# Kernel optimization log

Hardware: AMD Instinct MI355X
Metric: run time of the kernel (lower is better)

The kernel has to match this reference:

```python
import jax, jax.numpy as jnp
import numpy as np

N, D = 8192, 128

def setup_inputs() -> dict:
    key = jax.random.key(0)
    kq, kk, kv = jax.random.split(key, 3)
    query = jax.random.normal(kq, (N, D), dtype=jnp.float32)
    key_t = jax.random.normal(kk, (N, D), dtype=jnp.float32)
    value = jax.random.normal(kv, (N, D), dtype=jnp.float32)
    return {"query": query, "key": key_t, "value": value}

def reference(query, key, value):
    # FlashAttention-2 online softmax over blocks is mathematically exact
    # softmax attention: out = softmax(Q K^T / sqrt(d)) V, no mask.
    d = query.shape[-1]
    scale = 1.0 / jnp.sqrt(jnp.asarray(d, dtype=query.dtype))
    scores = jnp.einsum('qd,kd->qk', query, key) * scale  # [n, n]
    probs = jax.nn.softmax(scores, axis=-1)
    return jnp.einsum('qk,kd->qd', probs, value)  # [n, d]
```

## Files before the change

### kernel.cpp

```cpp
#include <hip/hip_runtime.h>
#include <hip/hip_bf16.h>

#define ATTN_N 8192
#define ATTN_D 128
#define TKEYS 128
#define NTILES (ATTN_N / TKEYS)
#define TILE_ELEMS (TKEYS * ATTN_D)
#define QROWS 64
#define KTPB 32

typedef __bf16 bf16_t;
typedef bf16_t bf16x2 __attribute__((ext_vector_type(2)));
typedef bf16_t bf16x8 __attribute__((ext_vector_type(8)));
typedef float f32x4 __attribute__((ext_vector_type(4)));

#if __has_builtin(__builtin_amdgcn_exp2f)
#define EXP2(x) __builtin_amdgcn_exp2f(x)
#else
#define EXP2(x) __expf((x) * 0.6931471805599453f)
#endif

__device__ __forceinline__ void dma16(const bf16_t* g, bf16_t* l) {
  __builtin_amdgcn_global_load_lds(
      (const __attribute__((address_space(1))) void*)g,
      (__attribute__((address_space(3))) void*)l, 16, 0, 0);
}

__global__ void prep_kernel(const float* __restrict__ q,
                            const float* __restrict__ k,
                            const float* __restrict__ v,
                            bf16_t* __restrict__ qb,
                            bf16_t* __restrict__ kswz,
                            bf16_t* __restrict__ vtswz) {
  __shared__ bf16_t tile[64][72];
  const int bk = blockIdx.x;
  const int bd = blockIdx.y;
  const int t = threadIdx.x;
  const float sc = 0.12751744f;

  const int row_l = t >> 2;
  const int key = bk * 64 + row_l;
  const int kt = key >> 7;
  const int r = key & 127;

#pragma unroll
  for (int u = 0; u < 2; ++u) {
    const int j = bd * 8 + (t & 3) * 2 + u;
    const float4* qs = (const float4*)(q + (size_t)key * ATTN_D + j * 8);
    const float4* ks = (const float4*)(k + (size_t)key * ATTN_D + j * 8);
    float4 a0 = qs[0], a1 = qs[1];
    float4 b0 = ks[0], b1 = ks[1];
    bf16x8 qo, ko;
    qo[0] = (bf16_t)(a0.x * sc); qo[1] = (bf16_t)(a0.y * sc);
    qo[2] = (bf16_t)(a0.z * sc); qo[3] = (bf16_t)(a0.w * sc);
    qo[4] = (bf16_t)(a1.x * sc); qo[5] = (bf16_t)(a1.y * sc);
    qo[6] = (bf16_t)(a1.z * sc); qo[7] = (bf16_t)(a1.w * sc);
    ko[0] = (bf16_t)b0.x; ko[1] = (bf16_t)b0.y;
    ko[2] = (bf16_t)b0.z; ko[3] = (bf16_t)b0.w;
    ko[4] = (bf16_t)b1.x; ko[5] = (bf16_t)b1.y;
    ko[6] = (bf16_t)b1.z; ko[7] = (bf16_t)b1.w;
    *(bf16x8*)(qb + (size_t)key * ATTN_D + j * 8) = qo;
    *(bf16x8*)(kswz + (size_t)kt * TILE_ELEMS + r * ATTN_D + (j ^ (r & 15)) * 8) = ko;
  }

  {
    const float* src = v + (size_t)key * ATTN_D + bd * 64 + (t & 3) * 16;
#pragma unroll
    for (int u = 0; u < 4; ++u) {
      float4 a = ((const float4*)src)[u];
      tile[row_l][(t & 3) * 16 + u * 4 + 0] = (bf16_t)a.x;
      tile[row_l][(t & 3) * 16 + u * 4 + 1] = (bf16_t)a.y;
      tile[row_l][(t & 3) * 16 + u * 4 + 2] = (bf16_t)a.z;
      tile[row_l][(t & 3) * 16 + u * 4 + 3] = (bf16_t)a.w;
    }
  }
  __syncthreads();
  {
    const int d_l = t >> 2;
    const int d = bd * 64 + d_l;
    const int h = bk & 1;
    const int ktv = bk >> 1;
#pragma unroll
    for (int u = 0; u < 2; ++u) {
      const int j = 8 * h + (t & 3) * 2 + u;
      bf16x8 o;
#pragma unroll
      for (int i = 0; i < 8; ++i) {
        const int key_tile = (j >> 2) * 32 + 4 * (j & 3) + (i >> 1) + 16 * (i & 1);
        o[i] = tile[key_tile - h * 64][d_l];
      }
      *(bf16x8*)(vtswz + (size_t)ktv * TILE_ELEMS + d * TKEYS + (j ^ (d & 15)) * 8) = o;
    }
  }
}

__global__ __launch_bounds__(512) void flash_attn_kernel(
    const bf16_t* __restrict__ qb, const bf16_t* __restrict__ kswz,
    const bf16_t* __restrict__ vtswz, float* __restrict__ partO,
    float* __restrict__ partL) {
  __shared__ __align__(16) bf16_t KV[2][2][TILE_ELEMS];
  __shared__ __align__(16) bf16_t Ps[8][32][40];
  __shared__ float cmb[8][32];
  float* Ob = (float*)&KV[0][0][0];

  const int t = threadIdx.x;
  const int w = t >> 6;
  const int lane = t & 63;
  const int quad = lane >> 4;
  const int col = lane & 15;
  const int rowHalf = w & 1;
  const int keyQ = w >> 1;
  const int blk = blockIdx.x;
  const int qg = blk >> 1;
  const int kh = blk & 1;
  const int q0 = qg * QROWS;
  const int ktbase = kh * KTPB;
  const int stg = ((blk >> 3) & 3) * 8;

  int offK[4][2], offV[8];
#pragma unroll
  for (int c = 0; c < 4; ++c)
#pragma unroll
    for (int cs = 0; cs < 2; ++cs)
      offK[c][cs] = (keyQ * 32 + cs * 16 + col) * ATTN_D +
                    (((c * 4 + quad) ^ col) * 8);
#pragma unroll
  for (int ds = 0; ds < 8; ++ds)
    offV[ds] = (ds * 16 + col) * TKEYS + (((keyQ * 4 + quad) ^ col) * 8);

  bf16x8 aq[2][4];
#pragma unroll
  for (int mi = 0; mi < 2; ++mi) {
    const int row = q0 + rowHalf * 32 + mi * 16 + col;
#pragma unroll
    for (int c = 0; c < 4; ++c)
      aq[mi][c] = *(const bf16x8*)(qb + (size_t)row * ATTN_D + c * 32 + quad * 8);
  }

  f32x4 oacc[2][8];
#pragma unroll
  for (int mi = 0; mi < 2; ++mi)
#pragma unroll
    for (int i = 0; i < 8; ++i) oacc[mi][i] = (f32x4){0.f, 0.f, 0.f, 0.f};
  float l_part[2][4] = {{0.f, 0.f, 0.f, 0.f}, {0.f, 0.f, 0.f, 0.f}};

  {
    const int kt = ktbase + (stg & (KTPB - 1));
    const bf16_t* kg = kswz + (size_t)kt * TILE_ELEMS + t * 8;
    const bf16_t* vg = vtswz + (size_t)kt * TILE_ELEMS + t * 8;
#pragma unroll
    for (int u = 0; u < 4; ++u) {
      dma16(kg + u * 4096, &KV[0][0][t * 8 + u * 4096]);
      dma16(vg + u * 4096, &KV[0][1][t * 8 + u * 4096]);
    }
  }
  __syncthreads();

  for (int it = 0; it < KTPB; ++it) {
    const int buf = it & 1;
    if (it + 1 < KTPB) {
      const int nt = ktbase + ((stg + it + 1) & (KTPB - 1));
      const bf16_t* kg = kswz + (size_t)nt * TILE_ELEMS + t * 8;
      const bf16_t* vg = vtswz + (size_t)nt * TILE_ELEMS + t * 8;
      bf16_t* kl = &KV[buf ^ 1][0][t * 8];
      bf16_t* vl = &KV[buf ^ 1][1][t * 8];
#pragma unroll
      for (int u = 0; u < 4; ++u) {
        dma16(kg + u * 4096, kl + u * 4096);
        dma16(vg + u * 4096, vl + u * 4096);
      }
    }
    const bf16_t* Kb = KV[buf][0];
    const bf16_t* Vb = KV[buf][1];

    f32x4 s[2][2];
#pragma unroll
    for (int mi = 0; mi < 2; ++mi)
#pragma unroll
      for (int ni = 0; ni < 2; ++ni) s[mi][ni] = (f32x4){0.f, 0.f, 0.f, 0.f};
#pragma unroll
    for (int c = 0; c < 4; ++c) {
      bf16x8 b0 = *(const bf16x8*)(Kb + offK[c][0]);
      bf16x8 b1 = *(const bf16x8*)(Kb + offK[c][1]);
      s[0][0] = __builtin_amdgcn_mfma_f32_16x16x32_bf16(aq[0][c], b0, s[0][0], 0, 0, 0);
      s[1][0] = __builtin_amdgcn_mfma_f32_16x16x32_bf16(aq[1][c], b0, s[1][0], 0, 0, 0);
      s[0][1] = __builtin_amdgcn_mfma_f32_16x16x32_bf16(aq[0][c], b1, s[0][1], 0, 0, 0);
      s[1][1] = __builtin_amdgcn_mfma_f32_16x16x32_bf16(aq[1][c], b1, s[1][1], 0, 0, 0);
    }

#pragma unroll
    for (int mi = 0; mi < 2; ++mi)
#pragma unroll
      for (int r = 0; r < 4; ++r) {
        float p0 = EXP2(s[mi][0][r]);
        float p1 = EXP2(s[mi][1][r]);
        l_part[mi][r] += p0 + p1;
        *(bf16x2*)&Ps[w][mi * 16 + quad * 4 + r][col * 2] =
            (bf16x2){(bf16_t)p0, (bf16_t)p1};
      }

    bf16x8 ap0 = *(const bf16x8*)&Ps[w][col][quad * 8];
    bf16x8 ap1 = *(const bf16x8*)&Ps[w][16 + col][quad * 8];
#pragma unroll
    for (int ds = 0; ds < 8; ++ds) {
      bf16x8 bv = *(const bf16x8*)(Vb + offV[ds]);
      oacc[0][ds] = __builtin_amdgcn_mfma_f32_16x16x32_bf16(ap0, bv, oacc[0][ds], 0, 0, 0);
      oacc[1][ds] = __builtin_amdgcn_mfma_f32_16x16x32_bf16(ap1, bv, oacc[1][ds], 0, 0, 0);
    }
    __syncthreads();
  }

#pragma unroll
  for (int mi = 0; mi < 2; ++mi)
#pragma unroll
    for (int r = 0; r < 4; ++r) {
      float v = l_part[mi][r];
#pragma unroll
      for (int off = 1; off < 16; off <<= 1)
        v += __shfl_xor(v, off, 64);
      if (col == 0) cmb[w][mi * 16 + quad * 4 + r] = v;
    }
  __syncthreads();
  if (t < QROWS) {
    const int rh = t >> 5, rl = t & 31;
    partL[(size_t)blk * QROWS + t] = cmb[rh][rl] + cmb[2 + rh][rl] +
                                     cmb[4 + rh][rl] + cmb[6 + rh][rl];
  }

#pragma unroll
  for (int p = 0; p < 4; ++p) {
    if (keyQ == p) {
#pragma unroll
      for (int mi = 0; mi < 2; ++mi)
#pragma unroll
        for (int ds = 0; ds < 8; ++ds)
#pragma unroll
          for (int r = 0; r < 4; ++r) {
            const int row = rowHalf * 32 + mi * 16 + quad * 4 + r;
            if (p == 0)
              Ob[row * 132 + ds * 16 + col] = oacc[mi][ds][r];
            else
              Ob[row * 132 + ds * 16 + col] += oacc[mi][ds][r];
          }
    }
    __syncthreads();
  }

  {
    float* dst = partO + (size_t)blk * (QROWS * ATTN_D);
    const int row = t >> 3;
    const int c0 = (t & 7) * 16;
#pragma unroll
    for (int u = 0; u < 4; ++u) {
      float4 vv = *(float4*)&Ob[row * 132 + c0 + u * 4];
      *(float4*)(dst + row * ATTN_D + c0 + u * 4) = vv;
    }
  }
}

__global__ void merge_kernel(const float* __restrict__ partO,
                             const float* __restrict__ partL,
                             float* __restrict__ out) {
  const int idx = blockIdx.x * blockDim.x + threadIdx.x;
  const int row = idx >> 5;
  const int gi = row >> 6;
  const int rl = row & 63;
  const int li = rl * 32 + (idx & 31);
  const float4* p0 = (const float4*)(partO + (size_t)(2 * gi) * (QROWS * ATTN_D));
  const float4* p1 = (const float4*)(partO + (size_t)(2 * gi + 1) * (QROWS * ATTN_D));
  const float invL = 1.0f / (partL[(size_t)(2 * gi) * QROWS + rl] +
                             partL[(size_t)(2 * gi + 1) * QROWS + rl]);
  float4 a = p0[li], b = p1[li], o;
  o.x = (a.x + b.x) * invL;
  o.y = (a.y + b.y) * invL;
  o.z = (a.z + b.z) * invL;
  o.w = (a.w + b.w) * invL;
  ((float4*)out)[idx] = o;
}

extern "C" void kernel_launch(void* const* d_in, const int* in_sizes, int n_in,
                              void* d_out, int out_size, void* d_ws, size_t ws_size,
                              hipStream_t stream) {
  const float* q = (const float*)d_in[0];
  const float* k = (const float*)d_in[1];
  const float* v = (const float*)d_in[2];
  float* out = (float*)d_out;

  bf16_t* qb = (bf16_t*)d_ws;
  bf16_t* kswz = qb + (size_t)ATTN_N * ATTN_D;
  bf16_t* vtswz = kswz + (size_t)ATTN_N * ATTN_D;
  float* partO = (float*)(vtswz + (size_t)ATTN_N * ATTN_D);
  float* partL = partO + (size_t)256 * QROWS * ATTN_D;

  prep_kernel<<<dim3(ATTN_N / 64, 2), 256, 0, stream>>>(q, k, v, qb, kswz, vtswz);
  flash_attn_kernel<<<256, 512, 0, stream>>>(qb, kswz, vtswz, partO, partL);
  merge_kernel<<<(ATTN_N * ATTN_D / 4) / 256, 256, 0, stream>>>(partO, partL, out);
}
```

Measured before the change: 123.4 us.

## Split keys four ways with 64-key tiles and per-wave 16-row query slices

The key range is now split across four blocks per query group instead of two, with smaller 64-key tiles, so the grid doubles to 512 blocks and per-block LDS shrinks. This allows several blocks per CU. Each wave now owns 16 query rows and half of each key tile. The K/V layouts are reswizzled to match the new tile size, and the merge kernel sums four partials. s_setprio is also raised around the MFMA sections. The intent is better occupancy and latency hiding. The cost is more partial-output traffic and more merge work.

```diff
diff --git a/kernel.cpp b/kernel.cpp
--- a/kernel.cpp
+++ b/kernel.cpp
@@ -3,11 +3,12 @@
 
 #define ATTN_N 8192
 #define ATTN_D 128
-#define TKEYS 128
+#define TKEYS 64
 #define NTILES (ATTN_N / TKEYS)
 #define TILE_ELEMS (TKEYS * ATTN_D)
 #define QROWS 64
-#define KTPB 32
+#define SPLITK 4
+#define KTPB (NTILES / SPLITK)
 
 typedef __bf16 bf16_t;
 typedef bf16_t bf16x2 __attribute__((ext_vector_type(2)));
@@ -40,8 +41,6 @@
 
   const int row_l = t >> 2;
   const int key = bk * 64 + row_l;
-  const int kt = key >> 7;
-  const int r = key & 127;
 
 #pragma unroll
   for (int u = 0; u < 2; ++u) {
@@ -60,7 +59,7 @@
     ko[4] = (bf16_t)b1.x; ko[5] = (bf16_t)b1.y;
     ko[6] = (bf16_t)b1.z; ko[7] = (bf16_t)b1.w;
     *(bf16x8*)(qb + (size_t)key * ATTN_D + j * 8) = qo;
-    *(bf16x8*)(kswz + (size_t)kt * TILE_ELEMS + r * ATTN_D + (j ^ (r & 15)) * 8) = ko;
+    *(bf16x8*)(kswz + (size_t)key * ATTN_D + ((j ^ (key & 15)) * 8)) = ko;
   }
 
   {
@@ -78,29 +77,28 @@
   {
     const int d_l = t >> 2;
     const int d = bd * 64 + d_l;
-    const int h = bk & 1;
-    const int ktv = bk >> 1;
 #pragma unroll
     for (int u = 0; u < 2; ++u) {
-      const int j = 8 * h + (t & 3) * 2 + u;
+      const int j = (t & 3) * 2 + u;
       bf16x8 o;
 #pragma unroll
       for (int i = 0; i < 8; ++i) {
-        const int key_tile = (j >> 2) * 32 + 4 * (j & 3) + (i >> 1) + 16 * (i & 1);
-        o[i] = tile[key_tile - h * 64][d_l];
+        const int kl_ = 32 * (j >> 2) + 4 * (j & 3) + (i >> 1) + 16 * (i & 1);
+        o[i] = tile[kl_][d_l];
       }
-      *(bf16x8*)(vtswz + (size_t)ktv * TILE_ELEMS + d * TKEYS + (j ^ (d & 15)) * 8) = o;
-    }
-  }
-}
-
-__global__ __launch_bounds__(512) void flash_attn_kernel(
+      *(bf16x8*)(vtswz + (size_t)bk * TILE_ELEMS + d * TKEYS +
+                 ((j ^ (d & 7)) * 8)) = o;
+    }
+  }
+}
+
+__global__ __launch_bounds__(512, 4) void flash_attn_kernel(
     const bf16_t* __restrict__ qb, const bf16_t* __restrict__ kswz,
     const bf16_t* __restrict__ vtswz, float* __restrict__ partO,
     float* __restrict__ partL) {
   __shared__ __align__(16) bf16_t KV[2][2][TILE_ELEMS];
-  __shared__ __align__(16) bf16_t Ps[8][32][40];
-  __shared__ float cmb[8][32];
+  __shared__ __align__(16) bf16_t Ps[8][16][40];
+  __shared__ float cmb[8][16];
   float* Ob = (float*)&KV[0][0][0];
 
   const int t = threadIdx.x;
@@ -108,11 +106,11 @@
   const int lane = t & 63;
   const int quad = lane >> 4;
   const int col = lane & 15;
-  const int rowHalf = w & 1;
-  const int keyQ = w >> 1;
+  const int rowQ = w & 3;
+  const int keyQ = w >> 2;
   const int blk = blockIdx.x;
-  const int qg = blk >> 1;
-  const int kh = blk & 1;
+  const int qg = blk >> 2;
+  const int kh = blk & 3;
   const int q0 = qg * QROWS;
   const int ktbase = kh * KTPB;
   const int stg = ((blk >> 3) & 3) * 8;
@@ -121,35 +119,32 @@
 #pragma unroll
   for (int c = 0; c < 4; ++c)
 #pragma unroll
-    for (int cs = 0; cs < 2; ++cs)
-      offK[c][cs] = (keyQ * 32 + cs * 16 + col) * ATTN_D +
+    for (int ni = 0; ni < 2; ++ni)
+      offK[c][ni] = (keyQ * 32 + ni * 16 + col) * ATTN_D +
                     (((c * 4 + quad) ^ col) * 8);
 #pragma unroll
   for (int ds = 0; ds < 8; ++ds)
-    offV[ds] = (ds * 16 + col) * TKEYS + (((keyQ * 4 + quad) ^ col) * 8);
-
-  bf16x8 aq[2][4];
-#pragma unroll
-  for (int mi = 0; mi < 2; ++mi) {
-    const int row = q0 + rowHalf * 32 + mi * 16 + col;
+    offV[ds] = (ds * 16 + col) * TKEYS + (((keyQ * 4 + quad) ^ (col & 7)) * 8);
+
+  bf16x8 aq[4];
+  {
+    const int row = q0 + rowQ * 16 + col;
 #pragma unroll
     for (int c = 0; c < 4; ++c)
-      aq[mi][c] = *(const bf16x8*)(qb + (size_t)row * ATTN_D + c * 32 + quad * 8);
-  }
-
-  f32x4 oacc[2][8];
-#pragma unroll
-  for (int mi = 0; mi < 2; ++mi)
-#pragma unroll
-    for (int i = 0; i < 8; ++i) oacc[mi][i] = (f32x4){0.f, 0.f, 0.f, 0.f};
-  float l_part[2][4] = {{0.f, 0.f, 0.f, 0.f}, {0.f, 0.f, 0.f, 0.f}};
+      aq[c] = *(const bf16x8*)(qb + (size_t)row * ATTN_D + c * 32 + quad * 8);
+  }
+
+  f32x4 oacc[8];
+#pragma unroll
+  for (int i = 0; i < 8; ++i) oacc[i] = (f32x4){0.f, 0.f, 0.f, 0.f};
+  float l_part[4] = {0.f, 0.f, 0.f, 0.f};
 
   {
     const int kt = ktbase + (stg & (KTPB - 1));
     const bf16_t* kg = kswz + (size_t)kt * TILE_ELEMS + t * 8;
     const bf16_t* vg = vtswz + (size_t)kt * TILE_ELEMS + t * 8;
 #pragma unroll
-    for (int u = 0; u < 4; ++u) {
+    for (int u = 0; u < 2; ++u) {
       dma16(kg + u * 4096, &KV[0][0][t * 8 + u * 4096]);
       dma16(vg + u * 4096, &KV[0][1][t * 8 + u * 4096]);
     }
@@ -165,7 +160,7 @@
       bf16_t* kl = &KV[buf ^ 1][0][t * 8];
       bf16_t* vl = &KV[buf ^ 1][1][t * 8];
 #pragma unroll
-      for (int u = 0; u < 4; ++u) {
+      for (int u = 0; u < 2; ++u) {
         dma16(kg + u * 4096, kl + u * 4096);
         dma16(vg + u * 4096, vl + u * 4096);
       }
@@ -173,75 +168,64 @@
     const bf16_t* Kb = KV[buf][0];
     const bf16_t* Vb = KV[buf][1];
 
-    f32x4 s[2][2];
-#pragma unroll
-    for (int mi = 0; mi < 2; ++mi)
-#pragma unroll
-      for (int ni = 0; ni < 2; ++ni) s[mi][ni] = (f32x4){0.f, 0.f, 0.f, 0.f};
+    f32x4 s0 = (f32x4){0.f, 0.f, 0.f, 0.f};
+    f32x4 s1 = (f32x4){0.f, 0.f, 0.f, 0.f};
+    __builtin_amdgcn_s_setprio(1);
 #pragma unroll
     for (int c = 0; c < 4; ++c) {
       bf16x8 b0 = *(const bf16x8*)(Kb + offK[c][0]);
       bf16x8 b1 = *(const bf16x8*)(Kb + offK[c][1]);
-      s[0][0] = __builtin_amdgcn_mfma_f32_16x16x32_bf16(aq[0][c], b0, s[0][0], 0, 0, 0);
-      s[1][0] = __builtin_amdgcn_mfma_f32_16x16x32_bf16(aq[1][c], b0, s[1][0], 0, 0, 0);
-      s[0][1] = __builtin_amdgcn_mfma_f32_16x16x32_bf16(aq[0][c], b1, s[0][1], 0, 0, 0);
-      s[1][1] = __builtin_amdgcn_mfma_f32_16x16x32_bf16(aq[1][c], b1, s[1][1], 0, 0, 0);
-    }
-
-#pragma unroll
-    for (int mi = 0; mi < 2; ++mi)
-#pragma unroll
-      for (int r = 0; r < 4; ++r) {
-        float p0 = EXP2(s[mi][0][r]);
-        float p1 = EXP2(s[mi][1][r]);
-        l_part[mi][r] += p0 + p1;
-        *(bf16x2*)&Ps[w][mi * 16 + quad * 4 + r][col * 2] =
-            (bf16x2){(bf16_t)p0, (bf16_t)p1};
-      }
-
-    bf16x8 ap0 = *(const bf16x8*)&Ps[w][col][quad * 8];
-    bf16x8 ap1 = *(const bf16x8*)&Ps[w][16 + col][quad * 8];
+      s0 = __builtin_amdgcn_mfma_f32_16x16x32_bf16(aq[c], b0, s0, 0, 0, 0);
+      s1 = __builtin_amdgcn_mfma_f32_16x16x32_bf16(aq[c], b1, s1, 0, 0, 0);
+    }
+    __builtin_amdgcn_s_setprio(0);
+
+#pragma unroll
+    for (int r = 0; r < 4; ++r) {
+      float p0 = EXP2(s0[r]);
+      float p1 = EXP2(s1[r]);
+      l_part[r] += p0 + p1;
+      *(bf16x2*)&Ps[w][quad * 4 + r][col * 2] = (bf16x2){(bf16_t)p0, (bf16_t)p1};
+    }
+
+    bf16x8 ap = *(const bf16x8*)&Ps[w][col][quad * 8];
+    __builtin_amdgcn_s_setprio(1);
 #pragma unroll
     for (int ds = 0; ds < 8; ++ds) {
       bf16x8 bv = *(const bf16x8*)(Vb + offV[ds]);
-      oacc[0][ds] = __builtin_amdgcn_mfma_f32_16x16x32_bf16(ap0, bv, oacc[0][ds], 0, 0, 0);
-      oacc[1][ds] = __builtin_amdgcn_mfma_f32_16x16x32_bf16(ap1, bv, oacc[1][ds], 0, 0, 0);
-    }
+      oacc[ds] = __builtin_amdgcn_mfma_f32_16x16x32_bf16(ap, bv, oacc[ds], 0, 0, 0);
+    }
+    __builtin_amdgcn_s_setprio(0);
     __syncthreads();
   }
 
 #pragma unroll
-  for (int mi = 0; mi < 2; ++mi)
-#pragma unroll
-    for (int r = 0; r < 4; ++r) {
-      float v = l_part[mi][r];
-#pragma unroll
-      for (int off = 1; off < 16; off <<= 1)
-        v += __shfl_xor(v, off, 64);
-      if (col == 0) cmb[w][mi * 16 + quad * 4 + r] = v;
-    }
+  for (int r = 0; r < 4; ++r) {
+    float v = l_part[r];
+#pragma unroll
+    for (int off = 1; off < 16; off <<= 1)
+      v += __shfl_xor(v, off, 64);
+    if (col == 0) cmb[w][quad * 4 + r] = v;
+  }
   __syncthreads();
   if (t < QROWS) {
-    const int rh = t >> 5, rl = t & 31;
-    partL[(size_t)blk * QROWS + t] = cmb[rh][rl] + cmb[2 + rh][rl] +
-                                     cmb[4 + rh][rl] + cmb[6 + rh][rl];
-  }
-
-#pragma unroll
-  for (int p = 0; p < 4; ++p) {
+    const int rq = t >> 4, rl = t & 15;
+    partL[(size_t)blk * QROWS + t] = cmb[rq][rl] + cmb[4 + rq][rl];
+  }
+
+#pragma unroll
+  for (int p = 0; p < 2; ++p) {
     if (keyQ == p) {
 #pragma unroll
-      for (int mi = 0; mi < 2; ++mi)
-#pragma unroll
-        for (int ds = 0; ds < 8; ++ds)
-#pragma unroll
-          for (int r = 0; r < 4; ++r) {
-            const int row = rowHalf * 32 + mi * 16 + quad * 4 + r;
-            if (p == 0)
-              Ob[row * 132 + ds * 16 + col] = oacc[mi][ds][r];
-            else
-              Ob[row * 132 + ds * 16 + col] += oacc[mi][ds][r];
-          }
+      for (int ds = 0; ds < 8; ++ds)
+#pragma unroll
+        for (int r = 0; r < 4; ++r) {
+          const int row = rowQ * 16 + quad * 4 + r;
+          if (p == 0)
+            Ob[row * 132 + ds * 16 + col] = oacc[ds][r];
+          else
+            Ob[row * 132 + ds * 16 + col] += oacc[ds][r];
+        }
     }
     __syncthreads();
   }
@@ -266,15 +250,19 @@
   const int gi = row >> 6;
   const int rl = row & 63;
   const int li = rl * 32 + (idx & 31);
-  const float4* p0 = (const float4*)(partO + (size_t)(2 * gi) * (QROWS * ATTN_D));
-  const float4* p1 = (const float4*)(partO + (size_t)(2 * gi + 1) * (QROWS * ATTN_D));
-  const float invL = 1.0f / (partL[(size_t)(2 * gi) * QROWS + rl] +
-                             partL[(size_t)(2 * gi + 1) * QROWS + rl]);
-  float4 a = p0[li], b = p1[li], o;
-  o.x = (a.x + b.x) * invL;
-  o.y = (a.y + b.y) * invL;
-  o.z = (a.z + b.z) * invL;
-  o.w = (a.w + b.w) * invL;
+  const float4* p0 = (const float4*)(partO + (size_t)(4 * gi + 0) * (QROWS * ATTN_D));
+  const float4* p1 = (const float4*)(partO + (size_t)(4 * gi + 1) * (QROWS * ATTN_D));
+  const float4* p2 = (const float4*)(partO + (size_t)(4 * gi + 2) * (QROWS * ATTN_D));
+  const float4* p3 = (const float4*)(partO + (size_t)(4 * gi + 3) * (QROWS * ATTN_D));
+  const float invL = 1.0f / (partL[(size_t)(4 * gi + 0) * QROWS + rl] +
+                             partL[(size_t)(4 * gi + 1) * QROWS + rl] +
+                             partL[(size_t)(4 * gi + 2) * QROWS + rl] +
+                             partL[(size_t)(4 * gi + 3) * QROWS + rl]);
+  float4 a = p0[li], b = p1[li], c = p2[li], d = p3[li], o;
+  o.x = (a.x + b.x + c.x + d.x) * invL;
+  o.y = (a.y + b.y + c.y + d.y) * invL;
+  o.z = (a.z + b.z + c.z + d.z) * invL;
+  o.w = (a.w + b.w + c.w + d.w) * invL;
   ((float4*)out)[idx] = o;
 }
 
@@ -290,9 +278,9 @@
   bf16_t* kswz = qb + (size_t)ATTN_N * ATTN_D;
   bf16_t* vtswz = kswz + (size_t)ATTN_N * ATTN_D;
   float* partO = (float*)(vtswz + (size_t)ATTN_N * ATTN_D);
-  float* partL = partO + (size_t)256 * QROWS * ATTN_D;
+  float* partL = partO + (size_t)512 * QROWS * ATTN_D;
 
   prep_kernel<<<dim3(ATTN_N / 64, 2), 256, 0, stream>>>(q, k, v, qb, kswz, vtswz);
-  flash_attn_kernel<<<256, 512, 0, stream>>>(qb, kswz, vtswz, partO, partL);
+  flash_attn_kernel<<<512, 512, 0, stream>>>(qb, kswz, vtswz, partO, partL);
   merge_kernel<<<(ATTN_N * ATTN_D / 4) / 256, 256, 0, stream>>>(partO, partL, out);
 }
```

Result: faster. 116.6 us (-5.5%).
